# Kernel tuning notes

Hardware: AMD Instinct MI355X
Metric: run time of the kernel (lower is better)

Reference implementation:

```python
import jax, jax.numpy as jnp
import numpy as np

D = 1024
H = 16
DK = D // H
E = 8
DFF = 4 * D
TOPK = 2
EPS = 1e-5


def setup_inputs() -> dict:
    key = jax.random.key(0)
    ks = jax.random.split(key, 16)
    s_in = 1.0 / np.sqrt(D)
    s_ff = 1.0 / np.sqrt(DFF)
    return {
        "x": jax.random.normal(ks[0], (2, 2048, D), dtype=jnp.float32),
        "ln1_g": jnp.ones((D,), jnp.float32),
        "ln1_b": jnp.zeros((D,), jnp.float32),
        "w_qkv": jax.random.normal(ks[1], (D, 3 * D), jnp.float32) * s_in,
        "b_qkv": jnp.zeros((3 * D,), jnp.float32),
        "w_o": jax.random.normal(ks[2], (D, D), jnp.float32) * s_in,
        "b_o": jnp.zeros((D,), jnp.float32),
        "ln2_g": jnp.ones((D,), jnp.float32),
        "ln2_b": jnp.zeros((D,), jnp.float32),
        "gate_w": jax.random.normal(ks[3], (D, E), jnp.float32) * s_in,
        "gate_b": jnp.zeros((E,), jnp.float32),
        "W1": jax.random.normal(ks[4], (E, D, DFF), jnp.float32) * s_in,
        "b1": jnp.zeros((E, DFF), jnp.float32),
        "W2": jax.random.normal(ks[5], (E, DFF, D), jnp.float32) * s_ff,
        "b2": jnp.zeros((E, D), jnp.float32),
    }


def _layernorm(x, g, b):
    m = jnp.mean(x, axis=-1, keepdims=True)
    v = jnp.mean(jnp.square(x - m), axis=-1, keepdims=True)
    return (x - m) * jax.lax.rsqrt(v + EPS) * g + b


def reference(x, ln1_g, ln1_b, w_qkv, b_qkv, w_o, b_o, ln2_g, ln2_b,
              gate_w, gate_b, W1, b1, W2, b2):
    B, S, _ = x.shape
    # --- attention (pre-LN, residual) ---
    h = _layernorm(x, ln1_g, ln1_b)
    qkv = h @ w_qkv + b_qkv                      # [B,S,3D]
    q, k, v = jnp.split(qkv, 3, axis=-1)
    q = q.reshape(B, S, H, DK)
    k = k.reshape(B, S, H, DK)
    v = v.reshape(B, S, H, DK)
    scores = jnp.einsum('bqhd,bkhd->bhqk', q, k) / np.sqrt(DK)
    attn = jax.nn.softmax(scores, axis=-1)
    o = jnp.einsum('bhqk,bkhd->bqhd', attn, v).reshape(B, S, D)
    x = x + o @ w_o + b_o
    # --- MoE (pre-LN, residual) ---
    h = _layernorm(x, ln2_g, ln2_b).reshape(B * S, D)   # [T,D]
    logits = h @ gate_w + gate_b                        # [T,E]
    topv, topi = jax.lax.top_k(logits, TOPK)            # [T,K]
    gw = jax.nn.softmax(topv, axis=-1)                  # [T,K]
    # per-token per-expert combine weight (0 if expert not selected)
    ew = jnp.sum(jax.nn.one_hot(topi, E, dtype=h.dtype) * gw[..., None], axis=1)  # [T,E]
    hid = jax.nn.relu(jnp.einsum('td,edf->etf', h, W1) + b1[:, None, :])  # [E,T,DFF]
    out_e = jnp.einsum('etf,efd->etd', hid, W2) + b2[:, None, :]          # [E,T,D]
    moe = jnp.einsum('etd,te->td', out_e, ew)
    return x + moe.reshape(B, S, D)
```

## Files before the change

kernel.cpp:

```cpp
#include <hip/hip_runtime.h>

#define TT 4096
#define SS 2048
#define DD 1024
#define NH 16
#define NE 8
#define DFFC 4096

typedef _Float16 h8  __attribute__((ext_vector_type(8)));
typedef _Float16 h4v __attribute__((ext_vector_type(4)));
typedef float    f4  __attribute__((ext_vector_type(4)));

typedef __attribute__((address_space(3))) void lds_void;
typedef __attribute__((address_space(1))) const void gbl_void;

__device__ __forceinline__ f4 mfma16(h8 a, h8 b, f4 c){
  return __builtin_amdgcn_mfma_f32_16x16x32_f16(a, b, c, 0, 0, 0);
}
__device__ __forceinline__ void fsplit(float x, _Float16& hi, _Float16& lo){
  _Float16 h = (_Float16)x; hi = h; lo = (_Float16)(x - (float)h);
}
__device__ __forceinline__ void gll16(const void* g, void* l){
  __builtin_amdgcn_global_load_lds((gbl_void*)g, (lds_void*)l, 16, 0, 0);
}

template<int SPLIT>
__global__ __launch_bounds__(256) void conv_t(
    const float* __restrict__ in, _Float16* __restrict__ oh, _Float16* __restrict__ ol,
    int K, int N)
{
  __shared__ float tile[32][33];
  const int n0 = blockIdx.x*32, k0 = blockIdx.y*32;
  const int tx = threadIdx.x & 31, ty = threadIdx.x >> 5;
  const float* inp = in + (size_t)blockIdx.z*K*N;
  #pragma unroll
  for (int j=0;j<4;++j)
    tile[ty+j*8][tx] = inp[(size_t)(k0+ty+j*8)*N + n0 + tx];
  __syncthreads();
  const size_t ob = (size_t)blockIdx.z*K*N;
  #pragma unroll
  for (int j=0;j<4;++j){
    float v = tile[tx][ty+j*8];
    size_t o = ob + (size_t)(n0+ty+j*8)*K + k0 + tx;
    if constexpr (SPLIT){ _Float16 hi,lo; fsplit(v,hi,lo); oh[o]=hi; ol[o]=lo; }
    else oh[o] = (_Float16)v;
  }
}

template<int MODE>
__global__ __launch_bounds__(256) void ln_kernel(
    const float* __restrict__ in, const float* __restrict__ g, const float* __restrict__ b,
    _Float16* __restrict__ outHi, _Float16* __restrict__ outLo)
{
  const int t = blockIdx.x, tid = threadIdx.x;
  f4 v = ((const f4*)(in + (size_t)t*DD))[tid];
  float s = v.x+v.y+v.z+v.w;
  float q = v.x*v.x+v.y*v.y+v.z*v.z+v.w*v.w;
  #pragma unroll
  for (int off=32; off; off>>=1){ s += __shfl_xor(s,off); q += __shfl_xor(q,off); }
  __shared__ float red[8];
  int wid = tid>>6, lane = tid&63;
  if (lane==0){ red[wid]=s; red[4+wid]=q; }
  __syncthreads();
  s = red[0]+red[1]+red[2]+red[3];
  q = red[4]+red[5]+red[6]+red[7];
  float mean = s * (1.0f/DD);
  float var  = q * (1.0f/DD) - mean*mean;
  float vv = var + 1e-5f;
  float r = rsqrtf(vv);
  r = r * (1.5f - 0.5f*vv*r*r);
  f4 gv = ((const f4*)g)[tid], bv = ((const f4*)b)[tid];
  #pragma unroll
  for (int j=0;j<4;++j){
    float y = (v[j]-mean)*r*gv[j] + bv[j];
    size_t o = (size_t)t*DD + tid*4 + j;
    if constexpr (MODE==0){ _Float16 hi,lo; fsplit(y,hi,lo); outHi[o]=hi; outLo[o]=lo; }
    else { outHi[o]=(_Float16)y; }
  }
}

template<int MODE>
__global__ __launch_bounds__(256,2) void gemm_split3(
    const _Float16* __restrict__ Ah, const _Float16* __restrict__ Al,
    const _Float16* __restrict__ Bh, const _Float16* __restrict__ Bl,
    const float* __restrict__ bias,
    _Float16* __restrict__ Chi, _Float16* __restrict__ Clo,
    float* __restrict__ Cf, const float* __restrict__ resid,
    int N, int K, int GM)
{
  __shared__ __align__(16) char smem[65536];
  const int tid = threadIdx.x, lane = tid&63, wid = tid>>6;
  const int l15 = lane&15, l4 = lane>>4;
  const int bid = blockIdx.x;
  const int c = bid & 7, rr = bid >> 3, mpx = GM >> 3;
  const int tm = (c*mpx + (rr % mpx))*128, tn = (rr / mpx)*128;

  const _Float16* sA[4]; const _Float16* sB[4];
  #pragma unroll
  for (int i=0;i<4;++i){
    int row = i*32 + (tid>>3);
    int s = (tid&7) ^ (row&7);
    int plane = s>>2, koff = (s&3)*8;
    sA[i] = (plane ? Al : Ah) + (size_t)(tm+row)*K + koff;
    sB[i] = (plane ? Bl : Bh) + (size_t)(tn+row)*K + koff;
  }
  int offAh[4], offAl[4], offBh[4], offBl[4];
  #pragma unroll
  for (int m=0;m<4;++m){
    int rowA = (wid>>1)*64 + m*16 + l15;
    offAh[m] = rowA*64 + ((l4 ^ (rowA&7))<<3);
    offAl[m] = rowA*64 + (((4|l4) ^ (rowA&7))<<3);
    int rowB = (wid&1)*64 + m*16 + l15;
    offBh[m] = rowB*64 + ((l4 ^ (rowB&7))<<3);
    offBl[m] = rowB*64 + (((4|l4) ^ (rowB&7))<<3);
  }
  #pragma unroll
  for (int i=0;i<4;++i){
    int L = i*4096 + tid*16;
    gll16(sA[i], smem + L);
    gll16(sB[i], smem + 16384 + L);
  }
  __syncthreads();
  f4 acc[4][4] = {};
  int cur = 0;
  for (int k0=0; k0<K; k0+=32){
    if (k0+32 < K){
      int nb = (cur^1)*32768;
      #pragma unroll
      for (int i=0;i<4;++i){
        int L = i*4096 + tid*16;
        gll16(sA[i]+k0+32, smem + nb + L);
        gll16(sB[i]+k0+32, smem + nb + 16384 + L);
      }
    }
    const _Float16* As = (const _Float16*)(smem + cur*32768);
    const _Float16* Bs = (const _Float16*)(smem + cur*32768 + 16384);
    h8 ah[4], al[4], bh4[4], bl4[4];
    #pragma unroll
    for (int m=0;m<4;++m){ ah[m] = *(const h8*)&As[offAh[m]]; al[m] = *(const h8*)&As[offAl[m]]; }
    #pragma unroll
    for (int n=0;n<4;++n){ bh4[n] = *(const h8*)&Bs[offBh[n]]; bl4[n] = *(const h8*)&Bs[offBl[n]]; }
    #pragma unroll
    for (int n=0;n<4;++n)
      #pragma unroll
      for (int m=0;m<4;++m){
        acc[m][n] = mfma16(ah[m], bh4[n], acc[m][n]);
        acc[m][n] = mfma16(ah[m], bl4[n], acc[m][n]);
        acc[m][n] = mfma16(al[m], bh4[n], acc[m][n]);
      }
    __syncthreads();
    cur ^= 1;
  }
  const int wm = (wid>>1)*64, wn = (wid&1)*64;
  #pragma unroll
  for (int n=0;n<4;++n){
    int col = tn + wn + n*16 + l15;
    float bv = bias[col];
    #pragma unroll
    for (int m=0;m<4;++m)
      #pragma unroll
      for (int r=0;r<4;++r){
        int rowg = tm + wm + m*16 + l4*4 + r;
        float vv = acc[m][n][r] + bv;
        size_t co = (size_t)rowg*N + col;
        if constexpr (MODE==0){ _Float16 hi,lo; fsplit(vv,hi,lo); Chi[co]=hi; Clo[co]=lo; }
        else { Cf[co] = vv + resid[co]; }
      }
  }
}

__global__ __launch_bounds__(256) void vt_kernel(
    const _Float16* __restrict__ qkvH, const _Float16* __restrict__ qkvL,
    _Float16* __restrict__ vtH, _Float16* __restrict__ vtL)
{
  __shared__ _Float16 TH[64*72], TL[64*72];
  const int tid = threadIdx.x;
  const int tt = blockIdx.x*64;
  const int bh = blockIdx.y;
  const int b = bh>>4, h = bh&15;
  const size_t t0 = (size_t)b*SS;
  #pragma unroll
  for (int p=0;p<2;++p){
    int t = p*32 + (tid>>3), d0 = (tid&7)*8;
    size_t g = (t0 + tt + t)*(size_t)3072 + 2048 + h*64 + d0;
    h8 vh = *(const h8*)(qkvH+g), vl = *(const h8*)(qkvL+g);
    int cp = ((t>>3) ^ (tid&7)) & 7;
    int base = cp*8 + (t&7);
    #pragma unroll
    for (int j=0;j<8;++j){ TH[(d0+j)*72 + base] = vh[j]; TL[(d0+j)*72 + base] = vl[j]; }
  }
  __syncthreads();
  int d = tid>>2, seg = tid&3;
  size_t ob = ((size_t)bh*64 + d)*2048 + tt;
  #pragma unroll
  for (int jj=0;jj<2;++jj){
    int cch = jj*4 + seg, cp = (cch ^ (d>>3)) & 7;
    h8 vh = *(const h8*)&TH[d*72 + cp*8];
    h8 vl = *(const h8*)&TL[d*72 + cp*8];
    *(h8*)(vtH + ob + cch*8) = vh;
    *(h8*)(vtL + ob + cch*8) = vl;
  }
}

__global__ __launch_bounds__(256,2) void attn_kernel(
    const _Float16* __restrict__ qkvH, const _Float16* __restrict__ qkvL,
    const _Float16* __restrict__ vtH, const _Float16* __restrict__ vtL,
    _Float16* __restrict__ oH, _Float16* __restrict__ oL)
{
  __shared__ __align__(16) _Float16 KsH[64*64], KsL[64*64], VsH[64*64], VsL[64*64];
  __shared__ __align__(16) _Float16 PsH[4][32*72], PsL[4][32*72];
  const int tid = threadIdx.x, lane = tid & 63, wid = tid >> 6;
  const int l15 = lane & 15, l4 = lane >> 4;
  const int qt = blockIdx.x, bh = blockIdx.y;
  const int b = bh >> 4, h = bh & 15;
  const size_t t0 = (size_t)b * SS;
  const int qbase = qt*128 + wid*32;

  const int srow = tid>>3;
  const int ss = (tid&7) ^ (srow&7);
  const _Float16* kH = qkvH + (t0 + srow)*(size_t)3072 + 1024 + h*64 + ss*8;
  const _Float16* kL = qkvL + (t0 + srow)*(size_t)3072 + 1024 + h*64 + ss*8;
  const _Float16* vH = vtH + ((size_t)bh*64 + srow)*2048 + ss*8;
  const _Float16* vL = vtL + ((size_t)bh*64 + srow)*2048 + ss*8;
  const int ldsL0 = tid*16;

  int offF[4][2];
  #pragma unroll
  for (int n=0;n<4;++n)
    #pragma unroll
    for (int ks=0;ks<2;++ks){
      int row = n*16 + l15;
      offF[n][ks] = row*64 + (((ks*4 + l4) ^ (row&7))<<3);
    }

  h8 qh[2][2], ql[2][2];
  #pragma unroll
  for (int m=0;m<2;++m)
    #pragma unroll
    for (int ks=0;ks<2;++ks){
      size_t go = (t0 + qbase + m*16 + l15)*(size_t)3072 + h*64 + ks*32 + l4*8;
      qh[m][ks] = *(const h8*)(qkvH + go);
      ql[m][ks] = *(const h8*)(qkvL + go);
    }

  f4 oacc[2][4] = {};
  float mrun[2][4], lrun[2][4];
  #pragma unroll
  for (int m=0;m<2;++m)
    #pragma unroll
    for (int r=0;r<4;++r){ mrun[m][r] = -1e30f; lrun[m][r]=0.f; }

  for (int kv=0; kv<SS; kv+=64){
    #pragma unroll
    for (int cc=0; cc<2; ++cc){
      size_t kgo = (size_t)(kv + cc*32)*3072;
      size_t vgo = (size_t)kv + (size_t)cc*32*2048;
      int L = cc*4096 + ldsL0;
      gll16(kH + kgo, (char*)KsH + L);
      gll16(kL + kgo, (char*)KsL + L);
      gll16(vH + vgo, (char*)VsH + L);
      gll16(vL + vgo, (char*)VsL + L);
    }
    __syncthreads();

    f4 s[2][4] = {};
    #pragma unroll
    for (int n=0;n<4;++n)
      #pragma unroll
      for (int ks=0;ks<2;++ks){
        h8 kh = *(const h8*)&KsH[offF[n][ks]];
        h8 kl = *(const h8*)&KsL[offF[n][ks]];
        #pragma unroll
        for (int m=0;m<2;++m){
          s[m][n] = mfma16(qh[m][ks], kh, s[m][n]);
          s[m][n] = mfma16(qh[m][ks], kl, s[m][n]);
          s[m][n] = mfma16(ql[m][ks], kh, s[m][n]);
        }
      }

    #pragma unroll
    for (int m=0;m<2;++m)
      #pragma unroll
      for (int r=0;r<4;++r){
        float mx = fmaxf(fmaxf(s[m][0][r], s[m][1][r]), fmaxf(s[m][2][r], s[m][3][r]));
        #pragma unroll
        for (int off=1; off<16; off<<=1) mx = fmaxf(mx, __shfl_xor(mx, off));
        float mn = fmaxf(mrun[m][r], mx);
        float alpha = __expf((mrun[m][r]-mn)*0.125f);
        mrun[m][r] = mn;
        float pv0 = __expf((s[m][0][r]-mn)*0.125f);
        float pv1 = __expf((s[m][1][r]-mn)*0.125f);
        float pv2 = __expf((s[m][2][r]-mn)*0.125f);
        float pv3 = __expf((s[m][3][r]-mn)*0.125f);
        float ps = pv0+pv1+pv2+pv3;
        #pragma unroll
        for (int off=1; off<16; off<<=1) ps += __shfl_xor(ps, off);
        lrun[m][r] = lrun[m][r]*alpha + ps;
        #pragma unroll
        for (int nd=0;nd<4;++nd) oacc[m][nd][r] *= alpha;
        int qr = m*16 + l4*4 + r;
        _Float16 ph, pl;
        fsplit(pv0, ph, pl); PsH[wid][qr*72 + l15]    = ph; PsL[wid][qr*72 + l15]    = pl;
        fsplit(pv1, ph, pl); PsH[wid][qr*72 + 16+l15] = ph; PsL[wid][qr*72 + 16+l15] = pl;
        fsplit(pv2, ph, pl); PsH[wid][qr*72 + 32+l15] = ph; PsL[wid][qr*72 + 32+l15] = pl;
        fsplit(pv3, ph, pl); PsH[wid][qr*72 + 48+l15] = ph; PsL[wid][qr*72 + 48+l15] = pl;
      }

    #pragma unroll
    for (int ks=0;ks<2;++ks){
      h8 aph[2], apl[2];
      #pragma unroll
      for (int m=0;m<2;++m){
        aph[m] = *(const h8*)&PsH[wid][(m*16+l15)*72 + ks*32 + l4*8];
        apl[m] = *(const h8*)&PsL[wid][(m*16+l15)*72 + ks*32 + l4*8];
      }
      #pragma unroll
      for (int nd=0;nd<4;++nd){
        h8 vh = *(const h8*)&VsH[offF[nd][ks]];
        h8 vl = *(const h8*)&VsL[offF[nd][ks]];
        #pragma unroll
        for (int m=0;m<2;++m){
          oacc[m][nd] = mfma16(aph[m], vh, oacc[m][nd]);
          oacc[m][nd] = mfma16(aph[m], vl, oacc[m][nd]);
          oacc[m][nd] = mfma16(apl[m], vh, oacc[m][nd]);
        }
      }
    }
    __syncthreads();
  }

  #pragma unroll
  for (int m=0;m<2;++m){
    #pragma unroll
    for (int r=0;r<4;++r){ lrun[m][r] = 1.f / lrun[m][r]; }
    #pragma unroll
    for (int nd=0;nd<4;++nd)
      #pragma unroll
      for (int r=0;r<4;++r){
        float vv = oacc[m][nd][r] * lrun[m][r];
        size_t go = (t0 + qbase + m*16 + l4*4 + r)*(size_t)DD + h*64 + nd*16 + l15;
        _Float16 hi, lo; fsplit(vv, hi, lo);
        oH[go] = hi; oL[go] = lo;
      }
  }
}

__global__ __launch_bounds__(64) void gate_kernel(
    const float* __restrict__ x1, const float* __restrict__ g, const float* __restrict__ bb,
    const float* __restrict__ gw, const float* __restrict__ gb,
    int* __restrict__ topi, float* __restrict__ topw, int* __restrict__ cnt)
{
  const int t = blockIdx.x, lane = threadIdx.x;
  f4 xv[4];
  float s=0.f, q=0.f;
  #pragma unroll
  for (int i=0;i<4;++i){
    xv[i] = ((const f4*)(x1 + (size_t)t*DD))[lane + i*64];
    #pragma unroll
    for (int j=0;j<4;++j){ s += xv[i][j]; q += xv[i][j]*xv[i][j]; }
  }
  #pragma unroll
  for (int off=32; off; off>>=1){ s += __shfl_xor(s,off); q += __shfl_xor(q,off); }
  float mean = s*(1.f/DD), var = q*(1.f/DD)-mean*mean, vv = var+1e-5f;
  float r = rsqrtf(vv); r = r*(1.5f-0.5f*vv*r*r);
  float acc[8] = {0,0,0,0,0,0,0,0};
  #pragma unroll
  for (int i=0;i<4;++i){
    f4 gv = ((const f4*)g)[lane+i*64], bv = ((const f4*)bb)[lane+i*64];
    #pragma unroll
    for (int j=0;j<4;++j){
      int d = (lane+i*64)*4 + j;
      float hv = (xv[i][j]-mean)*r*gv[j] + bv[j];
      const f4* gp = (const f4*)(gw + (size_t)d*8);
      f4 g0 = gp[0], g1 = gp[1];
      acc[0]+=hv*g0.x; acc[1]+=hv*g0.y; acc[2]+=hv*g0.z; acc[3]+=hv*g0.w;
      acc[4]+=hv*g1.x; acc[5]+=hv*g1.y; acc[6]+=hv*g1.z; acc[7]+=hv*g1.w;
    }
  }
  #pragma unroll
  for (int e=0;e<8;++e)
    #pragma unroll
    for (int off=32;off;off>>=1) acc[e]+=__shfl_xor(acc[e],off);
  if (lane==0){
    float lg[8];
    #pragma unroll
    for (int e=0;e<8;++e) lg[e]=acc[e]+gb[e];
    int i0=0; float v0=lg[0];
    #pragma unroll
    for (int e=1;e<8;++e) if (lg[e]>v0){ v0=lg[e]; i0=e; }
    int i1=-1; float v1=-1e30f;
    #pragma unroll
    for (int e=0;e<8;++e) if (e!=i0 && lg[e]>v1){ v1=lg[e]; i1=e; }
    float w0 = 1.f/(1.f+__expf(v1-v0));
    topi[2*t]=i0; topi[2*t+1]=i1;
    topw[2*t]=w0; topw[2*t+1]=1.f-w0;
    atomicAdd(&cnt[i0],1); atomicAdd(&cnt[i1],1);
  }
}

__global__ void scan_kernel(const int* __restrict__ cnt, int* __restrict__ offs,
                            int* __restrict__ cursor, int* __restrict__ pref1,
                            int* __restrict__ pref2){
  if (threadIdx.x==0){
    int s=0, t1=0, t2=0;
    for (int e=0;e<8;++e){
      offs[e]=s; s+=cnt[e];
      int mt = (cnt[e]+127)>>7;
      pref1[e]=t1; t1 += mt*(DFFC/128);
      pref2[e]=t2; t2 += mt*(DD/128);
    }
    offs[8]=s; pref1[8]=t1; pref2[8]=t2;
  }
  if (threadIdx.x<8) cursor[threadIdx.x]=0;
}

__global__ __launch_bounds__(256) void scatter_kernel(
    const int* __restrict__ topi, const int* __restrict__ offs, int* __restrict__ cursor,
    int* __restrict__ tokl, int* __restrict__ posof)
{
  int t = blockIdx.x*256 + threadIdx.x;
  #pragma unroll
  for (int k=0;k<2;++k){
    int e = topi[2*t+k];
    int p = atomicAdd(&cursor[e],1);
    int idx = offs[e]+p;
    tokl[idx]=t; posof[2*t+k]=idx;
  }
}

template<int GATHER>
__global__ __launch_bounds__(256,2) void gemm_ffn(
    const _Float16* __restrict__ A, const _Float16* __restrict__ Bw,
    const float* __restrict__ bias, _Float16* __restrict__ C,
    const int* __restrict__ tok, const int* __restrict__ offs,
    const int* __restrict__ pref, int N, int K)
{
  __shared__ __align__(16) char smem[65536];
  const int tid = threadIdx.x, lane = tid&63, wid = tid>>6;
  const int l15 = lane&15, l4 = lane>>4;
  const int wm = (wid>>1)*64, wn = (wid&1)*64;
  const int tot = pref[8];

  int offA[4][2], offB[4][2];
  #pragma unroll
  for (int m=0;m<4;++m)
    #pragma unroll
    for (int ks=0;ks<2;++ks){
      int rowA = wm + m*16 + l15;
      offA[m][ks] = rowA*64 + (((ks*4+l4) ^ (rowA&7))<<3);
      int rowB = wn + m*16 + l15;
      offB[m][ks] = rowB*64 + (((ks*4+l4) ^ (rowB&7))<<3);
    }

  for (int idx = blockIdx.x; idx < tot; idx += gridDim.x){
    int e = 0;
    #pragma unroll
    for (int k=1;k<8;++k) if (pref[k] <= idx) e = k;
    const int off = offs[e], Me = offs[e+1]-off;
    const int mt = (Me+127)>>7;
    const int local = idx - pref[e];
    const int ni = local / mt, mi = local - ni*mt;
    const int tm = mi*128, tn = ni*128;
    const _Float16* Bp = Bw + (size_t)e*N*K + (size_t)tn*K;
    const float* biasp = bias + (size_t)e*N;

    const _Float16* sA[4]; const _Float16* sB[4];
    #pragma unroll
    for (int i=0;i<4;++i){
      int row = i*32 + (tid>>3);
      int s = (tid&7) ^ (row&7);
      int lr = min(tm+row, Me-1);
      size_t ar = GATHER ? (size_t)tok[off+lr] : (size_t)(off+lr);
      sA[i] = A + ar*K + s*8;
      sB[i] = Bp + (size_t)row*K + s*8;
    }
    #pragma unroll
    for (int i=0;i<4;++i){
      int L = i*4096 + tid*16;
      gll16(sA[i], smem + L);
      gll16(sB[i], smem + 16384 + L);
    }
    __syncthreads();
    f4 acc[4][4] = {};
    int cur = 0;
    for (int k0=0; k0<K; k0+=64){
      if (k0+64 < K){
        int nb = (cur^1)*32768;
        #pragma unroll
        for (int i=0;i<4;++i){
          int L = i*4096 + tid*16;
          gll16(sA[i]+k0+64, smem + nb + L);
          gll16(sB[i]+k0+64, smem + nb + 16384 + L);
        }
      }
      const _Float16* As = (const _Float16*)(smem + cur*32768);
      const _Float16* Bs = (const _Float16*)(smem + cur*32768 + 16384);
      #pragma unroll
      for (int ks=0;ks<2;++ks){
        h8 av[4], bv[4];
        #pragma unroll
        for (int m=0;m<4;++m) av[m] = *(const h8*)&As[offA[m][ks]];
        #pragma unroll
        for (int n=0;n<4;++n) bv[n] = *(const h8*)&Bs[offB[n][ks]];
        #pragma unroll
        for (int n=0;n<4;++n)
          #pragma unroll
          for (int m=0;m<4;++m)
            acc[m][n] = mfma16(av[m], bv[n], acc[m][n]);
      }
      __syncthreads();
      cur ^= 1;
    }
    _Float16* Cs = (_Float16*)smem;
    float bvv[4];
    #pragma unroll
    for (int n=0;n<4;++n) bvv[n] = biasp[tn + wn + n*16 + l15];
    #pragma unroll
    for (int p=0;p<2;++p){
      if ((wid&1)==p){
        #pragma unroll
        for (int n=0;n<4;++n)
          #pragma unroll
          for (int m=0;m<4;++m)
            #pragma unroll
            for (int r=0;r<4;++r){
              int row = wm + m*16 + l4*4 + r;
              float vv = acc[m][n][r] + bvv[n];
              if constexpr (GATHER) vv = fmaxf(vv, 0.f);
              Cs[row*72 + n*16 + l15] = (_Float16)vv;
            }
      }
      __syncthreads();
      int row = tid>>1, seg = tid&1;
      if (tm+row < Me){
        size_t gb = (size_t)(off+tm+row)*N + tn + p*64 + seg*32;
        #pragma unroll
        for (int j=0;j<4;++j)
          *(h8*)(C + gb + j*8) = *(const h8*)&Cs[row*72 + seg*32 + j*8];
      }
      __syncthreads();
    }
  }
}

__global__ __launch_bounds__(256) void combine_kernel(
    const float* __restrict__ x1, const _Float16* __restrict__ moe,
    const float* __restrict__ topw, const int* __restrict__ posof, float* __restrict__ out)
{
  int t = blockIdx.x, tid = threadIdx.x;
  size_t o = (size_t)t*DD + tid*4;
  f4 xv = *(const f4*)(x1+o);
  int p0=posof[2*t], p1=posof[2*t+1];
  float w0=topw[2*t], w1=topw[2*t+1];
  h4v m0 = *(const h4v*)(moe + (size_t)p0*DD + tid*4);
  h4v m1 = *(const h4v*)(moe + (size_t)p1*DD + tid*4);
  f4 r;
  #pragma unroll
  for (int j=0;j<4;++j) r[j] = xv[j] + w0*(float)m0[j] + w1*(float)m1[j];
  *(f4*)(out+o) = r;
}

extern "C" void kernel_launch(void* const* d_in, const int* in_sizes, int n_in,
                              void* d_out, int out_size, void* d_ws, size_t ws_size,
                              hipStream_t stream)
{
  (void)in_sizes; (void)n_in; (void)out_size; (void)ws_size;
  const float* x     = (const float*)d_in[0];
  const float* ln1g  = (const float*)d_in[1];
  const float* ln1b  = (const float*)d_in[2];
  const float* wqkv  = (const float*)d_in[3];
  const float* bqkv  = (const float*)d_in[4];
  const float* wo    = (const float*)d_in[5];
  const float* bo    = (const float*)d_in[6];
  const float* ln2g  = (const float*)d_in[7];
  const float* ln2b  = (const float*)d_in[8];
  const float* gatew = (const float*)d_in[9];
  const float* gateb = (const float*)d_in[10];
  const float* W1    = (const float*)d_in[11];
  const float* b1    = (const float*)d_in[12];
  const float* W2    = (const float*)d_in[13];
  const float* b2    = (const float*)d_in[14];
  float* out = (float*)d_out;

  char* w = (char*)d_ws;
  _Float16* W1T    = (_Float16*)(w);
  _Float16* W2T    = (_Float16*)(w + 67108864);
  _Float16* wqT_H  = (_Float16*)(w + 134217728);
  _Float16* wqT_L  = (_Float16*)(w + 140509184);
  _Float16* woT_H  = (_Float16*)(w + 146800640);
  _Float16* woT_L  = (_Float16*)(w + 148897792);
  char* rb = w + 150994944;
  _Float16* h1H  = (_Float16*)(rb);
  _Float16* h1L  = (_Float16*)(rb + 8388608);
  _Float16* vtH  = (_Float16*)(rb);
  _Float16* vtL  = (_Float16*)(rb + 8388608);
  _Float16* qkvH = (_Float16*)(rb + 16777216);
  _Float16* qkvL = (_Float16*)(rb + 41943040);
  _Float16* hid  = (_Float16*)(rb);
  char* rm = w + 218103808;
  _Float16* oH  = (_Float16*)(rm);
  _Float16* oL  = (_Float16*)(rm + 8388608);
  _Float16* moe = (_Float16*)(rm);
  float* x1     = (float*)(w + 234881024);
  _Float16* h2h = (_Float16*)(w + 251658240);
  char* sm = w + 260046848;
  float* topw  = (float*)(sm);
  int*   topi  = (int*)(sm + 32768);
  int*   posof = (int*)(sm + 65536);
  int*   tokl  = (int*)(sm + 98304);
  int*   cnt   = (int*)(sm + 131072);
  int*   offs  = (int*)(sm + 131072 + 64);
  int*   cursor= (int*)(sm + 131072 + 128);
  int*   pref1 = (int*)(sm + 131072 + 192);
  int*   pref2 = (int*)(sm + 131072 + 256);

  conv_t<1><<<dim3(96, 32, 1),  256, 0, stream>>>(wqkv, wqT_H, wqT_L, 1024, 3072);
  conv_t<1><<<dim3(32, 32, 1),  256, 0, stream>>>(wo,   woT_H, woT_L, 1024, 1024);
  conv_t<0><<<dim3(128, 32, 8), 256, 0, stream>>>(W1, W1T, nullptr, 1024, 4096);
  conv_t<0><<<dim3(32, 128, 8), 256, 0, stream>>>(W2, W2T, nullptr, 4096, 1024);

  ln_kernel<0><<<TT, 256, 0, stream>>>(x, ln1g, ln1b, h1H, h1L);
  gemm_split3<0><<<768, 256, 0, stream>>>(
      h1H, h1L, wqT_H, wqT_L, bqkv, qkvH, qkvL, nullptr, nullptr, 3072, 1024, 32);
  vt_kernel<<<dim3(32, 32), 256, 0, stream>>>(qkvH, qkvL, vtH, vtL);
  attn_kernel<<<dim3(SS/128, 2*NH), 256, 0, stream>>>(qkvH, qkvL, vtH, vtL, oH, oL);
  gemm_split3<1><<<256, 256, 0, stream>>>(
      oH, oL, woT_H, woT_L, bo, nullptr, nullptr, x1, x, 1024, 1024, 32);
  ln_kernel<1><<<TT, 256, 0, stream>>>(x1, ln2g, ln2b, h2h, nullptr);
  hipMemsetAsync(cnt, 0, 8*sizeof(int), stream);
  gate_kernel<<<TT, 64, 0, stream>>>(x1, ln2g, ln2b, gatew, gateb, topi, topw, cnt);
  scan_kernel<<<1, 32, 0, stream>>>(cnt, offs, cursor, pref1, pref2);
  scatter_kernel<<<TT/256, 256, 0, stream>>>(topi, offs, cursor, tokl, posof);
  gemm_ffn<1><<<512, 256, 0, stream>>>(h2h, W1T, b1, hid, tokl, offs, pref1, DFFC, 1024);
  gemm_ffn<0><<<512, 256, 0, stream>>>(hid, W2T, b2, moe, tokl, offs, pref2, DD, DFFC);
  combine_kernel<<<TT, 256, 0, stream>>>(x1, moe, topw, posof, out);
}
```

Baseline: 849.5 us.

## Vectorize weight transpose with 64x64 tiles and register-prefetch attention K/V tiles

The weight conversion/transpose kernel now uses 64x64 tiles with float4 global loads and 8-wide half stores, cutting the number of memory instructions per element. The attention loop replaces direct global-to-LDS loads with a register-staged prefetch of the next K/V tile, issued after the LDS write so global latency overlaps the MFMA and softmax work. It also raises wave priority around the MFMA blocks. This costs more registers, which may reduce occupancy, and moves a barrier to the top of the loop.

```diff
diff --git a/kernel.cpp b/kernel.cpp
--- a/kernel.cpp
+++ b/kernel.cpp
@@ -29,21 +29,30 @@
     const float* __restrict__ in, _Float16* __restrict__ oh, _Float16* __restrict__ ol,
     int K, int N)
 {
-  __shared__ float tile[32][33];
-  const int n0 = blockIdx.x*32, k0 = blockIdx.y*32;
-  const int tx = threadIdx.x & 31, ty = threadIdx.x >> 5;
+  __shared__ float tile[64][65];
+  const int n0 = blockIdx.x*64, k0 = blockIdx.y*64;
+  const int tid = threadIdx.x;
   const float* inp = in + (size_t)blockIdx.z*K*N;
   #pragma unroll
-  for (int j=0;j<4;++j)
-    tile[ty+j*8][tx] = inp[(size_t)(k0+ty+j*8)*N + n0 + tx];
+  for (int p=0;p<4;++p){
+    int row = p*16 + (tid>>4), col4 = (tid&15)*4;
+    *(f4*)&tile[row][col4] = *(const f4*)(inp + (size_t)(k0+row)*N + n0 + col4);
+  }
   __syncthreads();
   const size_t ob = (size_t)blockIdx.z*K*N;
   #pragma unroll
-  for (int j=0;j<4;++j){
-    float v = tile[tx][ty+j*8];
-    size_t o = ob + (size_t)(n0+ty+j*8)*K + k0 + tx;
-    if constexpr (SPLIT){ _Float16 hi,lo; fsplit(v,hi,lo); oh[o]=hi; ol[o]=lo; }
-    else oh[o] = (_Float16)v;
+  for (int p=0;p<2;++p){
+    int n = p*32 + (tid>>3), k8 = (tid&7)*8;
+    h8 vh, vl;
+    #pragma unroll
+    for (int j=0;j<8;++j){
+      float v = tile[k8+j][n];
+      if constexpr (SPLIT){ _Float16 hi,lo; fsplit(v,hi,lo); vh[j]=hi; vl[j]=lo; }
+      else vh[j] = (_Float16)v;
+    }
+    size_t o = ob + (size_t)(n0+n)*K + k0 + k8;
+    *(h8*)(oh + o) = vh;
+    if constexpr (SPLIT) *(h8*)(ol + o) = vl;
   }
 }
 
@@ -250,20 +259,42 @@
     #pragma unroll
     for (int r=0;r<4;++r){ mrun[m][r] = -1e30f; lrun[m][r]=0.f; }
 
+  h8 rKH[2], rKL[2], rVH[2], rVL[2];
+  #pragma unroll
+  for (int cc=0; cc<2; ++cc){
+    size_t kgo = (size_t)(cc*32)*3072;
+    size_t vgo = (size_t)cc*32*2048;
+    rKH[cc] = *(const h8*)(kH + kgo);
+    rKL[cc] = *(const h8*)(kL + kgo);
+    rVH[cc] = *(const h8*)(vH + vgo);
+    rVL[cc] = *(const h8*)(vL + vgo);
+  }
+
   for (int kv=0; kv<SS; kv+=64){
+    __syncthreads();
     #pragma unroll
     for (int cc=0; cc<2; ++cc){
-      size_t kgo = (size_t)(kv + cc*32)*3072;
-      size_t vgo = (size_t)kv + (size_t)cc*32*2048;
       int L = cc*4096 + ldsL0;
-      gll16(kH + kgo, (char*)KsH + L);
-      gll16(kL + kgo, (char*)KsL + L);
-      gll16(vH + vgo, (char*)VsH + L);
-      gll16(vL + vgo, (char*)VsL + L);
+      *(h8*)((char*)KsH + L) = rKH[cc];
+      *(h8*)((char*)KsL + L) = rKL[cc];
+      *(h8*)((char*)VsH + L) = rVH[cc];
+      *(h8*)((char*)VsL + L) = rVL[cc];
     }
     __syncthreads();
+    if (kv+64 < SS){
+      #pragma unroll
+      for (int cc=0; cc<2; ++cc){
+        size_t kgo = (size_t)(kv+64 + cc*32)*3072;
+        size_t vgo = (size_t)(kv+64) + (size_t)cc*32*2048;
+        rKH[cc] = *(const h8*)(kH + kgo);
+        rKL[cc] = *(const h8*)(kL + kgo);
+        rVH[cc] = *(const h8*)(vH + vgo);
+        rVL[cc] = *(const h8*)(vL + vgo);
+      }
+    }
 
     f4 s[2][4] = {};
+    __builtin_amdgcn_s_setprio(1);
     #pragma unroll
     for (int n=0;n<4;++n)
       #pragma unroll
@@ -277,6 +308,7 @@
           s[m][n] = mfma16(ql[m][ks], kh, s[m][n]);
         }
       }
+    __builtin_amdgcn_s_setprio(0);
 
     #pragma unroll
     for (int m=0;m<2;++m)
@@ -306,6 +338,7 @@
         fsplit(pv3, ph, pl); PsH[wid][qr*72 + 48+l15] = ph; PsL[wid][qr*72 + 48+l15] = pl;
       }
 
+    __builtin_amdgcn_s_setprio(1);
     #pragma unroll
     for (int ks=0;ks<2;++ks){
       h8 aph[2], apl[2];
@@ -326,7 +359,7 @@
         }
       }
     }
-    __syncthreads();
+    __builtin_amdgcn_s_setprio(0);
   }
 
   #pragma unroll
@@ -614,10 +647,10 @@
   int*   pref1 = (int*)(sm + 131072 + 192);
   int*   pref2 = (int*)(sm + 131072 + 256);
 
-  conv_t<1><<<dim3(96, 32, 1),  256, 0, stream>>>(wqkv, wqT_H, wqT_L, 1024, 3072);
-  conv_t<1><<<dim3(32, 32, 1),  256, 0, stream>>>(wo,   woT_H, woT_L, 1024, 1024);
-  conv_t<0><<<dim3(128, 32, 8), 256, 0, stream>>>(W1, W1T, nullptr, 1024, 4096);
-  conv_t<0><<<dim3(32, 128, 8), 256, 0, stream>>>(W2, W2T, nullptr, 4096, 1024);
+  conv_t<1><<<dim3(48, 16, 1), 256, 0, stream>>>(wqkv, wqT_H, wqT_L, 1024, 3072);
+  conv_t<1><<<dim3(16, 16, 1), 256, 0, stream>>>(wo,   woT_H, woT_L, 1024, 1024);
+  conv_t<0><<<dim3(64, 16, 8), 256, 0, stream>>>(W1, W1T, nullptr, 1024, 4096);
+  conv_t<0><<<dim3(16, 64, 8), 256, 0, stream>>>(W2, W2T, nullptr, 4096, 1024);
 
   ln_kernel<0><<<TT, 256, 0, stream>>>(x, ln1g, ln1b, h1H, h1L);
   gemm_split3<0><<<768, 256, 0, stream>>>(
```

After: 843.0 us. Within noise of the previous version (-0.8%).
